# Performance work log

Measured on AMD Instinct MI355X. Metric: run time of the kernel, lower is better.

## Reference

```python
import jax, jax.numpy as jnp
import numpy as np

N_NODES = 100000
N_REL = 3
HID = 256
LN_EPS = 1e-5
DENOM_EPS = 1e-8


def setup_inputs() -> dict:
    key = jax.random.key(0)
    ks = jax.random.split(key, 8)
    E = 300000
    return {
        "feat_text": jax.random.normal(ks[0], (N_NODES, 384), dtype=jnp.float32),
        "feat_image": jax.random.normal(ks[1], (N_NODES, 512), dtype=jnp.float32),
        "W_text": jax.random.normal(ks[2], (384, HID), dtype=jnp.float32) * 0.05,
        "W_image": jax.random.normal(ks[3], (512, HID), dtype=jnp.float32) * 0.05,
        "W_rel": jax.random.normal(ks[4], (N_REL, HID, HID), dtype=jnp.float32) * 0.05,
        "ln_gamma": jnp.ones((HID,), dtype=jnp.float32),
        "ln_beta": jnp.zeros((HID,), dtype=jnp.float32),
        "edge_weight": jax.random.uniform(ks[5], (E,), dtype=jnp.float32),
        "edge_index": jax.random.randint(ks[6], (2, E), 0, N_NODES),
        "edge_type": jax.random.randint(ks[7], (E,), 0, N_REL),
    }


def _layer_norm(x, gamma, beta):
    mu = jnp.mean(x, axis=-1, keepdims=True)
    var = jnp.mean(jnp.square(x - mu), axis=-1, keepdims=True)
    return (x - mu) * jax.lax.rsqrt(var + LN_EPS) * gamma + beta


def reference(feat_text, feat_image, W_text, W_image, W_rel, ln_gamma, ln_beta,
              edge_weight, edge_index, edge_type):
    # base embedding: mean of per-modality projections (fuse_mode='avg'), node 0 zeroed
    h0 = 0.5 * (feat_text @ W_text + feat_image @ W_image)  # [N, H]
    h0 = h0.at[0].set(0.0)

    src = edge_index[0]
    dst = edge_index[1]
    h_src = h0[src]  # [E, H] gather once, reused per relation

    aggregated = jnp.zeros_like(h0)
    for rel in range(N_REL):  # small fixed relation count
        w = jnp.where(edge_type == rel, edge_weight, 0.0)          # [E]
        msgs = (h_src @ W_rel[rel]) * w[:, None]                    # [E, H]
        agg_rel = jax.ops.segment_sum(msgs, dst, num_segments=N_NODES)   # [N, H]
        denom = jax.ops.segment_sum(w, dst, num_segments=N_NODES)        # [N]
        aggregated = aggregated + agg_rel / jnp.maximum(denom, DENOM_EPS)[:, None]

    # dropout=0.0 (identity)
    h1 = _layer_norm(h0 + aggregated, ln_gamma, ln_beta)
    h1 = h1.at[0].set(0.0)
    return h1
```

## Files before the change

### kernel.cpp

```cpp
#include <hip/hip_runtime.h>
#include <hip/hip_bf16.h>

#define HID 256
#define LN_EPS 1e-5f
#define DENOM_EPS 1e-8f

typedef __attribute__((ext_vector_type(8))) short short8;
typedef __attribute__((ext_vector_type(4))) float f32x4;

#define WP1_ELEMS (28 * 256 * 32)
#define WP2_ELEMS (24 * 256 * 32)

__device__ inline unsigned bfpk(float x, float y) {
    __hip_bfloat162 h = __float22bfloat162_rn(make_float2(x, y));
    return *reinterpret_cast<unsigned*>(&h);
}

__device__ inline void gld16(const void* g, void* l) {
    __builtin_amdgcn_global_load_lds(
        (const __attribute__((address_space(1))) void*)g,
        (__attribute__((address_space(3))) void*)l, 16, 0, 0);
}

__global__ __launch_bounds__(256) void kpack(
    const float* __restrict__ wt, const float* __restrict__ wi,
    const float* __restrict__ wrel,
    __hip_bfloat16* __restrict__ wp1, __hip_bfloat16* __restrict__ wp2)
{
    int idx = blockIdx.x * 256 + threadIdx.x;
    if (idx < WP1_ELEMS) {
        int kk = idx & 31, col = (idx >> 5) & 255, ks = idx >> 13;
        int k = ks * 32 + kk;
        float v = (k < 384) ? wt[k * 256 + col] : wi[(k - 384) * 256 + col];
        wp1[idx] = __float2bfloat16(v * 0.5f);
    } else {
        int j = idx - WP1_ELEMS;
        if (j < WP2_ELEMS) {
            int kk = j & 31, col = (j >> 5) & 255, ks = j >> 13;
            int k = ks * 32 + kk;
            wp2[j] = __float2bfloat16(wrel[k * 256 + col]);
        }
    }
}

__global__ __launch_bounds__(256) void kchain(
    const int* __restrict__ edst, int* __restrict__ head, int* __restrict__ nxt, int E)
{
    int e = blockIdx.x * 256 + threadIdx.x;
    if (e < E) nxt[e] = atomicExch(&head[edst[e]], e);
}

__global__ __launch_bounds__(256) void k2_gather(
    const float* __restrict__ h0, const int* __restrict__ esrc,
    const int* __restrict__ etype, const float* __restrict__ ew,
    const int* __restrict__ head, const int* __restrict__ nxt,
    __hip_bfloat16* __restrict__ S, int N)
{
    int gid = blockIdx.x * 256 + threadIdx.x;
    int d = gid >> 6;
    int lane = gid & 63;
    if (d >= N) return;

    f32x4 a0 = {0.f, 0.f, 0.f, 0.f}, a1 = a0, a2 = a0;
    float d0 = 0.f, d1 = 0.f, d2 = 0.f;

    int e = head[d];
    while (e >= 0) {
        int src = esrc[e];
        int ty = etype[e];
        float w = ew[e];
        const float4 h = *(const float4*)(h0 + (size_t)src * HID + lane * 4);
        f32x4 hw = {w * h.x, w * h.y, w * h.z, w * h.w};
        if (ty == 0)      { a0 += hw; d0 += w; }
        else if (ty == 1) { a1 += hw; d1 += w; }
        else              { a2 += hw; d2 += w; }
        e = nxt[e];
    }

    float i0 = 1.0f / fmaxf(d0, DENOM_EPS);
    float i1 = 1.0f / fmaxf(d1, DENOM_EPS);
    float i2 = 1.0f / fmaxf(d2, DENOM_EPS);
    __hip_bfloat16* row = S + (size_t)d * 768;
    uint2 p;
    p = make_uint2(bfpk(a0[0] * i0, a0[1] * i0), bfpk(a0[2] * i0, a0[3] * i0));
    *(uint2*)(row + 0   + lane * 4) = p;
    p = make_uint2(bfpk(a1[0] * i1, a1[1] * i1), bfpk(a1[2] * i1, a1[3] * i1));
    *(uint2*)(row + 256 + lane * 4) = p;
    p = make_uint2(bfpk(a2[0] * i2, a2[1] * i2), bfpk(a2[2] * i2, a2[3] * i2));
    *(uint2*)(row + 512 + lane * 4) = p;
}

template<int MODE>
__global__ __launch_bounds__(256, 4) void kgemm(
    const float* __restrict__ a0, const float* __restrict__ a1,
    const __hip_bfloat16* __restrict__ Sb,
    const __hip_bfloat16* __restrict__ wp,
    const float* h0in, const float* __restrict__ gamma,
    const float* __restrict__ beta, float* out, int N)
{
    constexpr int NSTEPS = MODE ? 24 : 28;
    constexpr int TB = MODE ? 4096 : 8192;
    __shared__ __align__(16) unsigned char As[3][TB];
    __shared__ float redS[MODE ? 64 : 1][4];
    __shared__ float redQ[MODE ? 64 : 1][4];

    const int t = threadIdx.x;
    const int lane = t & 63;
    const int w = t >> 6;
    const int m0 = blockIdx.x * 64;
    const int g = lane >> 4;

    auto stageA = [&](int ks, int buf) {
        if constexpr (MODE == 0) {
#pragma unroll
            for (int j = 0; j < 2; ++j) {
                int slot = j * 4 + w;
                int r = slot * 8 + (lane >> 3);
                int grow = m0 + r; if (grow >= N) grow = m0;
                int q = (lane & 7) ^ (lane >> 3);
                const float* src = (ks < 12)
                    ? (a0 + (size_t)grow * 384 + ks * 32 + q * 4)
                    : (a1 + (size_t)grow * 512 + (ks - 12) * 32 + q * 4);
                gld16(src, As[buf] + slot * 1024);
            }
        } else {
            int r = w * 16 + (lane >> 2);
            int grow = m0 + r; if (grow >= N) grow = m0;
            int q = (lane & 3) ^ ((lane >> 3) & 3);
            const __hip_bfloat16* src = Sb + (size_t)grow * 768 + ks * 32 + q * 8;
            gld16(src, As[buf] + w * 1024);
        }
    };
    auto loadB = [&](short8 (&bf)[4], int ks) {
#pragma unroll
        for (int fc = 0; fc < 4; ++fc)
            bf[fc] = *(const short8*)((const short*)wp +
                      (size_t)(ks * 256 + w * 64 + fc * 16 + (lane & 15)) * 32 + g * 8);
    };

    f32x4 acc[4][4];
#pragma unroll
    for (int i = 0; i < 4; ++i)
#pragma unroll
        for (int j = 0; j < 4; ++j) acc[i][j] = (f32x4){0.f, 0.f, 0.f, 0.f};

    auto compute = [&](int ks, short8 (&bf)[4]) {
        const unsigned char* Ab = As[ks % 3];
        short8 af[4];
#pragma unroll
        for (int fr = 0; fr < 4; ++fr) {
            int r = fr * 16 + (lane & 15);
            if constexpr (MODE == 0) {
                const unsigned char* base = Ab + r * 128;
                f32x4 lo = *(const f32x4*)(base + ((2 * g) ^ (r & 7)) * 16);
                f32x4 hi = *(const f32x4*)(base + ((2 * g + 1) ^ (r & 7)) * 16);
                union { short8 s; unsigned u[4]; } cv;
                cv.u[0] = bfpk(lo[0], lo[1]);
                cv.u[1] = bfpk(lo[2], lo[3]);
                cv.u[2] = bfpk(hi[0], hi[1]);
                cv.u[3] = bfpk(hi[2], hi[3]);
                af[fr] = cv.s;
            } else {
                af[fr] = *(const short8*)(Ab + r * 64 + (g ^ ((r >> 1) & 3)) * 16);
            }
        }
#pragma unroll
        for (int fr = 0; fr < 4; ++fr)
#pragma unroll
            for (int fc = 0; fc < 4; ++fc)
                acc[fr][fc] = __builtin_amdgcn_mfma_f32_16x16x32_bf16(af[fr], bf[fc], acc[fr][fc], 0, 0, 0);
    };

    short8 bfe[4], bfo[4];

    stageA(0, 0);
    stageA(1, 1);
    loadB(bfe, 0);

    constexpr int NP = NSTEPS / 2;
    for (int p = 0; p < NP; ++p) {
        const int ks = 2 * p;
        if constexpr (MODE == 0) asm volatile("s_waitcnt vmcnt(6)" ::: "memory");
        else                     asm volatile("s_waitcnt vmcnt(5)" ::: "memory");
        __builtin_amdgcn_s_barrier();
        if (ks + 2 < NSTEPS) stageA(ks + 2, (ks + 2) % 3);
        loadB(bfo, ks + 1);
        compute(ks, bfe);
        if (p == NP - 1)              asm volatile("s_waitcnt vmcnt(0)" ::: "memory");
        else if constexpr (MODE == 0) asm volatile("s_waitcnt vmcnt(6)" ::: "memory");
        else                          asm volatile("s_waitcnt vmcnt(5)" ::: "memory");
        __builtin_amdgcn_s_barrier();
        if (ks + 3 < NSTEPS) stageA(ks + 3, (ks + 3) % 3);
        if (ks + 2 < NSTEPS) loadB(bfe, ks + 2);
        compute(ks + 1, bfo);
    }

    const int cbase = w * 64;

    if constexpr (MODE == 0) {
#pragma unroll
        for (int fr = 0; fr < 4; ++fr)
#pragma unroll
            for (int reg = 0; reg < 4; ++reg) {
                int grow = m0 + fr * 16 + g * 4 + reg;
                if (grow >= N) continue;
#pragma unroll
                for (int fc = 0; fc < 4; ++fc) {
                    float vv = acc[fr][fc][reg];
                    if (grow == 0) vv = 0.f;
                    out[(size_t)grow * 256 + cbase + fc * 16 + (lane & 15)] = vv;
                }
            }
    } else {
#pragma unroll
        for (int fr = 0; fr < 4; ++fr)
#pragma unroll
            for (int reg = 0; reg < 4; ++reg) {
                int grow = m0 + fr * 16 + g * 4 + reg;
                if (grow < N) {
#pragma unroll
                    for (int fc = 0; fc < 4; ++fc)
                        acc[fr][fc][reg] += h0in[(size_t)grow * 256 + cbase + fc * 16 + (lane & 15)];
                }
            }
#pragma unroll
        for (int fr = 0; fr < 4; ++fr)
#pragma unroll
            for (int reg = 0; reg < 4; ++reg) {
                float s = 0.f, q = 0.f;
#pragma unroll
                for (int fc = 0; fc < 4; ++fc) {
                    float vv = acc[fr][fc][reg];
                    s += vv; q += vv * vv;
                }
#pragma unroll
                for (int off = 1; off < 16; off <<= 1) {
                    s += __shfl_xor(s, off, 64);
                    q += __shfl_xor(q, off, 64);
                }
                if ((lane & 15) == 0) {
                    int rl = fr * 16 + g * 4 + reg;
                    redS[rl][w] = s;
                    redQ[rl][w] = q;
                }
            }
        __syncthreads();
        float g4[4], b4[4];
#pragma unroll
        for (int fc = 0; fc < 4; ++fc) {
            g4[fc] = gamma[cbase + fc * 16 + (lane & 15)];
            b4[fc] = beta[cbase + fc * 16 + (lane & 15)];
        }
#pragma unroll
        for (int fr = 0; fr < 4; ++fr)
#pragma unroll
            for (int reg = 0; reg < 4; ++reg) {
                int rl = fr * 16 + g * 4 + reg;
                int grow = m0 + rl;
                if (grow >= N) continue;
                float s = redS[rl][0] + redS[rl][1] + redS[rl][2] + redS[rl][3];
                float q = redQ[rl][0] + redQ[rl][1] + redQ[rl][2] + redQ[rl][3];
                float mu  = s * (1.f / 256.f);
                float var = q * (1.f / 256.f) - mu * mu;
                float rstd = rsqrtf(var + LN_EPS);
#pragma unroll
                for (int fc = 0; fc < 4; ++fc) {
                    float vv = (acc[fr][fc][reg] - mu) * rstd * g4[fc] + b4[fc];
                    if (grow == 0) vv = 0.f;
                    out[(size_t)grow * 256 + cbase + fc * 16 + (lane & 15)] = vv;
                }
            }
    }
}

extern "C" void kernel_launch(void* const* d_in, const int* in_sizes, int n_in,
                              void* d_out, int out_size, void* d_ws, size_t ws_size,
                              hipStream_t stream) {
    const int N = in_sizes[0] / 384;
    const int E = in_sizes[7];
    const float* ft    = (const float*)d_in[0];
    const float* fi    = (const float*)d_in[1];
    const float* wt    = (const float*)d_in[2];
    const float* wi    = (const float*)d_in[3];
    const float* wrel  = (const float*)d_in[4];
    const float* gamma = (const float*)d_in[5];
    const float* beta  = (const float*)d_in[6];
    const float* ew    = (const float*)d_in[7];
    const int*   eidx  = (const int*)d_in[8];
    const int*   etype = (const int*)d_in[9];
    float* out = (float*)d_out;

    __hip_bfloat16* S = (__hip_bfloat16*)d_ws;
    int* head = (int*)((char*)d_ws + (size_t)N * 768 * 2);
    int* nxt  = head + N;
    __hip_bfloat16* wp1 = (__hip_bfloat16*)(nxt + E);
    __hip_bfloat16* wp2 = wp1 + WP1_ELEMS;

    hipMemsetAsync(head, 0xFF, (size_t)N * sizeof(int), stream);

    kpack<<<(WP1_ELEMS + WP2_ELEMS + 255) / 256, 256, 0, stream>>>(wt, wi, wrel, wp1, wp2);

    kchain<<<(E + 255) / 256, 256, 0, stream>>>(eidx + E, head, nxt, E);

    const int gblocks = (N + 63) / 64;
    kgemm<0><<<gblocks, 256, 0, stream>>>(ft, fi, nullptr, wp1, nullptr, nullptr, nullptr, out, N);

    const int wblocks = (N + 3) / 4;
    k2_gather<<<wblocks, 256, 0, stream>>>(out, eidx, etype, ew, head, nxt, S, N);

    kgemm<1><<<gblocks, 256, 0, stream>>>(nullptr, nullptr, S, wp2, out, gamma, beta, out, N);
}
```

Baseline: 323.0 us.

## Store base embedding in bf16 and add XCD-aware block swizzle to GEMMs

Measured after the change: 382.6 us. +18.5%, slower.

```diff
diff --git a/kernel.cpp b/kernel.cpp
--- a/kernel.cpp
+++ b/kernel.cpp
@@ -20,6 +20,22 @@
     __builtin_amdgcn_global_load_lds(
         (const __attribute__((address_space(1))) void*)g,
         (__attribute__((address_space(3))) void*)l, 16, 0, 0);
+}
+
+__device__ inline f32x4 bf4_to_f32(uint2 p) {
+    union { float f; unsigned u; } c;
+    f32x4 r;
+    c.u = (p.x & 0xFFFFu) << 16;  r[0] = c.f;
+    c.u = (p.x & 0xFFFF0000u);    r[1] = c.f;
+    c.u = (p.y & 0xFFFFu) << 16;  r[2] = c.f;
+    c.u = (p.y & 0xFFFF0000u);    r[3] = c.f;
+    return r;
+}
+
+__device__ inline int xcd_swz(int b, int nwg) {
+    int q = nwg >> 3, r = nwg & 7;
+    int xcd = b & 7, idx = b >> 3;
+    return (xcd < r) ? (xcd * (q + 1) + idx) : (r * (q + 1) + (xcd - r) * q + idx);
 }
 
 __global__ __launch_bounds__(256) void kpack(
@@ -50,15 +66,15 @@
     if (e < E) nxt[e] = atomicExch(&head[edst[e]], e);
 }
 
-__global__ __launch_bounds__(256) void k2_gather(
-    const float* __restrict__ h0, const int* __restrict__ esrc,
+__global__ __launch_bounds__(512) void k2_gather(
+    const __hip_bfloat16* __restrict__ h0b, const int* __restrict__ esrc,
     const int* __restrict__ etype, const float* __restrict__ ew,
     const int* __restrict__ head, const int* __restrict__ nxt,
     __hip_bfloat16* __restrict__ S, int N)
 {
-    int gid = blockIdx.x * 256 + threadIdx.x;
-    int d = gid >> 6;
-    int lane = gid & 63;
+    int w = threadIdx.x >> 6;
+    int lane = threadIdx.x & 63;
+    int d = blockIdx.x * 8 + w;
     if (d >= N) return;
 
     f32x4 a0 = {0.f, 0.f, 0.f, 0.f}, a1 = a0, a2 = a0;
@@ -68,12 +84,12 @@
     while (e >= 0) {
         int src = esrc[e];
         int ty = etype[e];
-        float w = ew[e];
-        const float4 h = *(const float4*)(h0 + (size_t)src * HID + lane * 4);
-        f32x4 hw = {w * h.x, w * h.y, w * h.z, w * h.w};
-        if (ty == 0)      { a0 += hw; d0 += w; }
-        else if (ty == 1) { a1 += hw; d1 += w; }
-        else              { a2 += hw; d2 += w; }
+        float we = ew[e];
+        uint2 hv = *(const uint2*)(h0b + (size_t)src * HID + lane * 4);
+        f32x4 h = bf4_to_f32(hv);
+        if (ty == 0)      { a0 += we * h; d0 += we; }
+        else if (ty == 1) { a1 += we * h; d1 += we; }
+        else              { a2 += we * h; d2 += we; }
         e = nxt[e];
     }
 
@@ -90,52 +106,39 @@
     *(uint2*)(row + 512 + lane * 4) = p;
 }
 
-template<int MODE>
-__global__ __launch_bounds__(256, 4) void kgemm(
-    const float* __restrict__ a0, const float* __restrict__ a1,
-    const __hip_bfloat16* __restrict__ Sb,
+__global__ __launch_bounds__(256, 4) void kg0(
+    const float* __restrict__ ft, const float* __restrict__ fi,
     const __hip_bfloat16* __restrict__ wp,
-    const float* h0in, const float* __restrict__ gamma,
-    const float* __restrict__ beta, float* out, int N)
-{
-    constexpr int NSTEPS = MODE ? 24 : 28;
-    constexpr int TB = MODE ? 4096 : 8192;
-    __shared__ __align__(16) unsigned char As[3][TB];
-    __shared__ float redS[MODE ? 64 : 1][4];
-    __shared__ float redQ[MODE ? 64 : 1][4];
+    __hip_bfloat16* __restrict__ h0b, int N, int nwg)
+{
+    constexpr int NSTEPS = 28;
+    __shared__ __align__(16) unsigned char As[3][8192];
 
     const int t = threadIdx.x;
     const int lane = t & 63;
     const int w = t >> 6;
-    const int m0 = blockIdx.x * 64;
+    const int m0 = xcd_swz(blockIdx.x, nwg) * 64;
     const int g = lane >> 4;
+    const int rl = lane & 15;
 
     auto stageA = [&](int ks, int buf) {
-        if constexpr (MODE == 0) {
-#pragma unroll
-            for (int j = 0; j < 2; ++j) {
-                int slot = j * 4 + w;
-                int r = slot * 8 + (lane >> 3);
-                int grow = m0 + r; if (grow >= N) grow = m0;
-                int q = (lane & 7) ^ (lane >> 3);
-                const float* src = (ks < 12)
-                    ? (a0 + (size_t)grow * 384 + ks * 32 + q * 4)
-                    : (a1 + (size_t)grow * 512 + (ks - 12) * 32 + q * 4);
-                gld16(src, As[buf] + slot * 1024);
-            }
-        } else {
-            int r = w * 16 + (lane >> 2);
+#pragma unroll
+        for (int j = 0; j < 2; ++j) {
+            int slot = j * 4 + w;
+            int r = slot * 8 + (lane >> 3);
             int grow = m0 + r; if (grow >= N) grow = m0;
-            int q = (lane & 3) ^ ((lane >> 3) & 3);
-            const __hip_bfloat16* src = Sb + (size_t)grow * 768 + ks * 32 + q * 8;
-            gld16(src, As[buf] + w * 1024);
+            int q = (lane & 7) ^ (lane >> 3);
+            const float* src = (ks < 12)
+                ? (ft + (size_t)grow * 384 + ks * 32 + q * 4)
+                : (fi + (size_t)grow * 512 + (ks - 12) * 32 + q * 4);
+            gld16(src, As[buf] + slot * 1024);
         }
     };
     auto loadB = [&](short8 (&bf)[4], int ks) {
 #pragma unroll
         for (int fc = 0; fc < 4; ++fc)
             bf[fc] = *(const short8*)((const short*)wp +
-                      (size_t)(ks * 256 + w * 64 + fc * 16 + (lane & 15)) * 32 + g * 8);
+                      (size_t)(ks * 256 + w * 64 + fc * 16 + rl) * 32 + g * 8);
     };
 
     f32x4 acc[4][4];
@@ -149,20 +152,16 @@
         short8 af[4];
 #pragma unroll
         for (int fr = 0; fr < 4; ++fr) {
-            int r = fr * 16 + (lane & 15);
-            if constexpr (MODE == 0) {
-                const unsigned char* base = Ab + r * 128;
-                f32x4 lo = *(const f32x4*)(base + ((2 * g) ^ (r & 7)) * 16);
-                f32x4 hi = *(const f32x4*)(base + ((2 * g + 1) ^ (r & 7)) * 16);
-                union { short8 s; unsigned u[4]; } cv;
-                cv.u[0] = bfpk(lo[0], lo[1]);
-                cv.u[1] = bfpk(lo[2], lo[3]);
-                cv.u[2] = bfpk(hi[0], hi[1]);
-                cv.u[3] = bfpk(hi[2], hi[3]);
-                af[fr] = cv.s;
-            } else {
-                af[fr] = *(const short8*)(Ab + r * 64 + (g ^ ((r >> 1) & 3)) * 16);
-            }
+            int r = fr * 16 + rl;
+            const unsigned char* base = Ab + r * 128;
+            f32x4 lo = *(const f32x4*)(base + ((2 * g) ^ (r & 7)) * 16);
+            f32x4 hi = *(const f32x4*)(base + ((2 * g + 1) ^ (r & 7)) * 16);
+            union { short8 s8; unsigned u[4]; } cv;
+            cv.u[0] = bfpk(lo[0], lo[1]);
+            cv.u[1] = bfpk(lo[2], lo[3]);
+            cv.u[2] = bfpk(hi[0], hi[1]);
+            cv.u[3] = bfpk(hi[2], hi[3]);
+            af[fr] = cv.s8;
         }
 #pragma unroll
         for (int fr = 0; fr < 4; ++fr)
@@ -172,105 +171,183 @@
     };
 
     short8 bfe[4], bfo[4];
-
     stageA(0, 0);
     stageA(1, 1);
     loadB(bfe, 0);
 
     constexpr int NP = NSTEPS / 2;
+#pragma unroll 1
     for (int p = 0; p < NP; ++p) {
         const int ks = 2 * p;
-        if constexpr (MODE == 0) asm volatile("s_waitcnt vmcnt(6)" ::: "memory");
-        else                     asm volatile("s_waitcnt vmcnt(5)" ::: "memory");
+        asm volatile("s_waitcnt vmcnt(6)" ::: "memory");
         __builtin_amdgcn_s_barrier();
+        __builtin_amdgcn_sched_barrier(0);
         if (ks + 2 < NSTEPS) stageA(ks + 2, (ks + 2) % 3);
         loadB(bfo, ks + 1);
         compute(ks, bfe);
-        if (p == NP - 1)              asm volatile("s_waitcnt vmcnt(0)" ::: "memory");
-        else if constexpr (MODE == 0) asm volatile("s_waitcnt vmcnt(6)" ::: "memory");
-        else                          asm volatile("s_waitcnt vmcnt(5)" ::: "memory");
+        if (p == NP - 1) asm volatile("s_waitcnt vmcnt(0)" ::: "memory");
+        else             asm volatile("s_waitcnt vmcnt(6)" ::: "memory");
         __builtin_amdgcn_s_barrier();
+        __builtin_amdgcn_sched_barrier(0);
         if (ks + 3 < NSTEPS) stageA(ks + 3, (ks + 3) % 3);
         if (ks + 2 < NSTEPS) loadB(bfe, ks + 2);
         compute(ks + 1, bfo);
     }
 
     const int cbase = w * 64;
-
-    if constexpr (MODE == 0) {
+#pragma unroll
+    for (int fr = 0; fr < 4; ++fr)
+#pragma unroll
+        for (int reg = 0; reg < 4; ++reg) {
+            int grow = m0 + fr * 16 + g * 4 + reg;
+            if (grow >= N) continue;
+#pragma unroll
+            for (int fc = 0; fc < 4; ++fc) {
+                float vv = acc[fr][fc][reg];
+                if (grow == 0) vv = 0.f;
+                h0b[(size_t)grow * 256 + cbase + fc * 16 + rl] = __float2bfloat16(vv);
+            }
+        }
+}
+
+__global__ __launch_bounds__(256, 4) void kg1(
+    const __hip_bfloat16* __restrict__ Sb,
+    const __hip_bfloat16* __restrict__ wp,
+    const __hip_bfloat16* __restrict__ h0b,
+    const float* __restrict__ gamma, const float* __restrict__ beta,
+    float* __restrict__ out, int N, int nwg)
+{
+    constexpr int NSTEPS = 24;
+    __shared__ __align__(16) unsigned char As[3][4096];
+    __shared__ float redS[64][4];
+    __shared__ float redQ[64][4];
+
+    const int t = threadIdx.x;
+    const int lane = t & 63;
+    const int w = t >> 6;
+    const int m0 = xcd_swz(blockIdx.x, nwg) * 64;
+    const int g = lane >> 4;
+    const int rl = lane & 15;
+
+    auto stageA = [&](int ks, int buf) {
+        int r = w * 16 + (lane >> 2);
+        int grow = m0 + r; if (grow >= N) grow = m0;
+        int q = (lane & 3) ^ ((lane >> 3) & 3);
+        const __hip_bfloat16* src = Sb + (size_t)grow * 768 + ks * 32 + q * 8;
+        gld16(src, As[buf] + w * 1024);
+    };
+    auto loadB = [&](short8 (&bf)[4], int ks) {
+#pragma unroll
+        for (int fc = 0; fc < 4; ++fc)
+            bf[fc] = *(const short8*)((const short*)wp +
+                      (size_t)(ks * 256 + w * 64 + fc * 16 + rl) * 32 + g * 8);
+    };
+
+    f32x4 acc[4][4];
+#pragma unroll
+    for (int i = 0; i < 4; ++i)
+#pragma unroll
+        for (int j = 0; j < 4; ++j) acc[i][j] = (f32x4){0.f, 0.f, 0.f, 0.f};
+
+    auto compute = [&](int ks, short8 (&bf)[4]) {
+        const unsigned char* Ab = As[ks % 3];
+        short8 af[4];
+#pragma unroll
+        for (int fr = 0; fr < 4; ++fr) {
+            int r = fr * 16 + rl;
+            af[fr] = *(const short8*)(Ab + r * 64 + (g ^ ((r >> 1) & 3)) * 16);
+        }
 #pragma unroll
         for (int fr = 0; fr < 4; ++fr)
 #pragma unroll
-            for (int reg = 0; reg < 4; ++reg) {
-                int grow = m0 + fr * 16 + g * 4 + reg;
-                if (grow >= N) continue;
-#pragma unroll
-                for (int fc = 0; fc < 4; ++fc) {
-                    float vv = acc[fr][fc][reg];
-                    if (grow == 0) vv = 0.f;
-                    out[(size_t)grow * 256 + cbase + fc * 16 + (lane & 15)] = vv;
-                }
-            }
-    } else {
-#pragma unroll
-        for (int fr = 0; fr < 4; ++fr)
-#pragma unroll
-            for (int reg = 0; reg < 4; ++reg) {
-                int grow = m0 + fr * 16 + g * 4 + reg;
-                if (grow < N) {
-#pragma unroll
-                    for (int fc = 0; fc < 4; ++fc)
-                        acc[fr][fc][reg] += h0in[(size_t)grow * 256 + cbase + fc * 16 + (lane & 15)];
-                }
-            }
-#pragma unroll
-        for (int fr = 0; fr < 4; ++fr)
-#pragma unroll
-            for (int reg = 0; reg < 4; ++reg) {
-                float s = 0.f, q = 0.f;
-#pragma unroll
-                for (int fc = 0; fc < 4; ++fc) {
-                    float vv = acc[fr][fc][reg];
-                    s += vv; q += vv * vv;
-                }
-#pragma unroll
-                for (int off = 1; off < 16; off <<= 1) {
-                    s += __shfl_xor(s, off, 64);
-                    q += __shfl_xor(q, off, 64);
-                }
-                if ((lane & 15) == 0) {
-                    int rl = fr * 16 + g * 4 + reg;
-                    redS[rl][w] = s;
-                    redQ[rl][w] = q;
-                }
-            }
-        __syncthreads();
-        float g4[4], b4[4];
-#pragma unroll
-        for (int fc = 0; fc < 4; ++fc) {
-            g4[fc] = gamma[cbase + fc * 16 + (lane & 15)];
-            b4[fc] = beta[cbase + fc * 16 + (lane & 15)];
-        }
-#pragma unroll
-        for (int fr = 0; fr < 4; ++fr)
-#pragma unroll
-            for (int reg = 0; reg < 4; ++reg) {
-                int rl = fr * 16 + g * 4 + reg;
-                int grow = m0 + rl;
-                if (grow >= N) continue;
-                float s = redS[rl][0] + redS[rl][1] + redS[rl][2] + redS[rl][3];
-                float q = redQ[rl][0] + redQ[rl][1] + redQ[rl][2] + redQ[rl][3];
-                float mu  = s * (1.f / 256.f);
-                float var = q * (1.f / 256.f) - mu * mu;
-                float rstd = rsqrtf(var + LN_EPS);
-#pragma unroll
-                for (int fc = 0; fc < 4; ++fc) {
-                    float vv = (acc[fr][fc][reg] - mu) * rstd * g4[fc] + b4[fc];
-                    if (grow == 0) vv = 0.f;
-                    out[(size_t)grow * 256 + cbase + fc * 16 + (lane & 15)] = vv;
-                }
-            }
-    }
+            for (int fc = 0; fc < 4; ++fc)
+                acc[fr][fc] = __builtin_amdgcn_mfma_f32_16x16x32_bf16(af[fr], bf[fc], acc[fr][fc], 0, 0, 0);
+    };
+
+    short8 bfe[4], bfo[4];
+    stageA(0, 0);
+    stageA(1, 1);
+    loadB(bfe, 0);
+
+    constexpr int NP = NSTEPS / 2;
+#pragma unroll 1
+    for (int p = 0; p < NP; ++p) {
+        const int ks = 2 * p;
+        asm volatile("s_waitcnt vmcnt(5)" ::: "memory");
+        __builtin_amdgcn_s_barrier();
+        __builtin_amdgcn_sched_barrier(0);
+        if (ks + 2 < NSTEPS) stageA(ks + 2, (ks + 2) % 3);
+        loadB(bfo, ks + 1);
+        compute(ks, bfe);
+        if (p == NP - 1) asm volatile("s_waitcnt vmcnt(0)" ::: "memory");
+        else             asm volatile("s_waitcnt vmcnt(5)" ::: "memory");
+        __builtin_amdgcn_s_barrier();
+        __builtin_amdgcn_sched_barrier(0);
+        if (ks + 3 < NSTEPS) stageA(ks + 3, (ks + 3) % 3);
+        if (ks + 2 < NSTEPS) loadB(bfe, ks + 2);
+        compute(ks + 1, bfo);
+    }
+
+    const int cbase = w * 64;
+#pragma unroll
+    for (int fr = 0; fr < 4; ++fr)
+#pragma unroll
+        for (int reg = 0; reg < 4; ++reg) {
+            int grow = m0 + fr * 16 + g * 4 + reg;
+            if (grow < N) {
+#pragma unroll
+                for (int fc = 0; fc < 4; ++fc)
+                    acc[fr][fc][reg] +=
+                        __bfloat162float(h0b[(size_t)grow * 256 + cbase + fc * 16 + rl]);
+            }
+        }
+#pragma unroll
+    for (int fr = 0; fr < 4; ++fr)
+#pragma unroll
+        for (int reg = 0; reg < 4; ++reg) {
+            float s = 0.f, q = 0.f;
+#pragma unroll
+            for (int fc = 0; fc < 4; ++fc) {
+                float vv = acc[fr][fc][reg];
+                s += vv; q += vv * vv;
+            }
+#pragma unroll
+            for (int off = 1; off < 16; off <<= 1) {
+                s += __shfl_xor(s, off, 64);
+                q += __shfl_xor(q, off, 64);
+            }
+            if (rl == 0) {
+                int rli = fr * 16 + g * 4 + reg;
+                redS[rli][w] = s;
+                redQ[rli][w] = q;
+            }
+        }
+    __syncthreads();
+    float g4[4], b4[4];
+#pragma unroll
+    for (int fc = 0; fc < 4; ++fc) {
+        g4[fc] = gamma[cbase + fc * 16 + rl];
+        b4[fc] = beta[cbase + fc * 16 + rl];
+    }
+#pragma unroll
+    for (int fr = 0; fr < 4; ++fr)
+#pragma unroll
+        for (int reg = 0; reg < 4; ++reg) {
+            int rli = fr * 16 + g * 4 + reg;
+            int grow = m0 + rli;
+            if (grow >= N) continue;
+            float s = redS[rli][0] + redS[rli][1] + redS[rli][2] + redS[rli][3];
+            float q = redQ[rli][0] + redQ[rli][1] + redQ[rli][2] + redQ[rli][3];
+            float mu  = s * (1.f / 256.f);
+            float var = q * (1.f / 256.f) - mu * mu;
+            float rstd = rsqrtf(var + LN_EPS);
+#pragma unroll
+            for (int fc = 0; fc < 4; ++fc) {
+                float vv = (acc[fr][fc][reg] - mu) * rstd * g4[fc] + b4[fc];
+                if (grow == 0) vv = 0.f;
+                out[(size_t)grow * 256 + cbase + fc * 16 + rl] = vv;
+            }
+        }
 }
 
 extern "C" void kernel_launch(void* const* d_in, const int* in_sizes, int n_in,
@@ -290,8 +367,9 @@
     const int*   etype = (const int*)d_in[9];
     float* out = (float*)d_out;
 
-    __hip_bfloat16* S = (__hip_bfloat16*)d_ws;
-    int* head = (int*)((char*)d_ws + (size_t)N * 768 * 2);
+    __hip_bfloat16* S   = (__hip_bfloat16*)d_ws;
+    __hip_bfloat16* h0b = S + (size_t)N * 768;
+    int* head = (int*)(h0b + (size_t)N * 256);
     int* nxt  = head + N;
     __hip_bfloat16* wp1 = (__hip_bfloat16*)(nxt + E);
     __hip_bfloat16* wp2 = wp1 + WP1_ELEMS;
@@ -303,10 +381,9 @@
     kchain<<<(E + 255) / 256, 256, 0, stream>>>(eidx + E, head, nxt, E);
 
     const int gblocks = (N + 63) / 64;
-    kgemm<0><<<gblocks, 256, 0, stream>>>(ft, fi, nullptr, wp1, nullptr, nullptr, nullptr, out, N);
-
-    const int wblocks = (N + 3) / 4;
-    k2_gather<<<wblocks, 256, 0, stream>>>(out, eidx, etype, ew, head, nxt, S, N);
-
-    kgemm<1><<<gblocks, 256, 0, stream>>>(nullptr, nullptr, S, wp2, out, gamma, beta, out, N);
-}
+    kg0<<<gblocks, 256, 0, stream>>>(ft, fi, wp1, h0b, N, gblocks);
+
+    k2_gather<<<(N + 7) / 8, 512, 0, stream>>>(h0b, eidx, etype, ew, head, nxt, S, N);
+
+    kg1<<<gblocks, 256, 0, stream>>>(S, wp2, h0b, gamma, beta, out, N, gblocks);
+}
```
